# Performance work log

Hardware: AMD Instinct MI355X
Metric: run time of the kernel (lower is better)

Reference implementation:

```python
import jax, jax.numpy as jnp
import numpy as np

_CODESZ = 8   # E8 codeword dimension
_OFFSET = 0.25  # half-integer shift applied to D8 points


def _build_grid():
    # Faithful replication of get_grid(): cartesian product of arange(-4,4)
    # over 8 dims (torch.cartesian_prod order == 'ij' meshgrid, last dim fastest),
    # keep points with even coordinate sum and squared norm <= 10 (D8 subset),
    # then concat [d8 - 1/4, d8 + 1/4]. Yields 55650 codewords of dim 8.
    rng = np.arange(-4, 4, dtype=np.int8)
    pts = np.stack(np.meshgrid(*([rng] * _CODESZ), indexing='ij'), axis=-1).reshape(-1, _CODESZ)
    s = pts.sum(axis=-1, dtype=np.int16)
    n2 = (pts.astype(np.int16) * pts).sum(axis=-1)  # max 8*16 fits int16
    d8 = pts[(s % 2 == 0) & (n2 <= 10)].astype(np.float32)  # [27825, 8]
    grid = np.concatenate([d8 - _OFFSET, d8 + _OFFSET], axis=0)  # [55650, 8]
    grid_norm = (grid * grid).sum(axis=-1)  # diag(grid @ grid.T), [55650]
    return jnp.asarray(grid), jnp.asarray(grid_norm)


def setup_inputs() -> dict:
    key = jax.random.key(0)
    X = jax.random.normal(key, (8192, _CODESZ), dtype=jnp.float32)
    grid, grid_norm = _build_grid()
    return {"X": X, "grid": grid, "grid_norm": grid_norm}


def reference(X, grid, grid_norm):
    # quantize(X, return_idx=True):
    # nearest codeword under L2 <=> argmax of 2*X@g - ||g||^2
    scores = 2.0 * (X @ grid.T) - grid_norm          # [N, 55650]
    idx = jnp.argmax(scores, axis=-1)                # [N]
    vals = jnp.take(grid, idx, axis=0)               # [N, 8]
    idx_i16 = (idx + (-2 ** 15)).astype(jnp.int16)   # idx_offset + int16 cast
    return vals, idx_i16
```

## Files before the change

### kernel.cpp

```cpp
#include <hip/hip_runtime.h>
#include <math.h>


typedef short short8 __attribute__((ext_vector_type(8)));
typedef float f32x16 __attribute__((ext_vector_type(16)));

constexpr int NROWS  = 8192;
constexpr int NCW    = 55650;
constexpr int NT     = 1740;
constexpr int NCWP   = NT * 32;
constexpr int NCHUNK = 24;
constexpr int RBLK   = 32;

constexpr size_t OFF_GB = 0;
constexpr size_t OFF_XS = OFF_GB + (size_t)NCWP * 32;
constexpr size_t OFF_BK = OFF_XS + (size_t)NROWS * 64;

__device__ inline unsigned short bf16_rne(float f) {
  unsigned int u = __float_as_uint(f);
  unsigned int r = u + 0x7FFFu + ((u >> 16) & 1u);
  return (unsigned short)(r >> 16);
}
__device__ inline float bf16_f(unsigned short h) {
  return __uint_as_float(((unsigned int)h) << 16);
}
__device__ inline unsigned int enc_ord(float f) {
  unsigned int u = __float_as_uint(f);
  return (u & 0x80000000u) ? ~u : (u | 0x80000000u);
}
__device__ inline float dec_ord(unsigned int e) {
  unsigned int u = (e & 0x80000000u) ? (e & 0x7FFFFFFFu) : ~e;
  return __uint_as_float(u);
}
__device__ inline float max16(const f32x16& d) {
  float t1 = fmaxf(fmaxf(d[0], d[1]), d[2]);
  float t2 = fmaxf(fmaxf(d[3], d[4]), d[5]);
  float t3 = fmaxf(fmaxf(d[6], d[7]), d[8]);
  float t4 = fmaxf(fmaxf(d[9], d[10]), d[11]);
  float t5 = fmaxf(fmaxf(d[12], d[13]), d[14]);
  float u1 = fmaxf(fmaxf(t1, t2), t3);
  float u2 = fmaxf(fmaxf(t4, t5), d[15]);
  return fmaxf(u1, u2);
}

__global__ __launch_bounds__(256) void e8_prep(
    const float* __restrict__ X, const float* __restrict__ G,
    const float* __restrict__ GN, unsigned short* __restrict__ Gb,
    unsigned short* __restrict__ Xs, unsigned long long* __restrict__ best) {
  int i = blockIdx.x * 256 + threadIdx.x;
  if (i < NCWP) {
    unsigned short g16[16];
    if (i < NCW) {
      for (int j = 0; j < 8; ++j) g16[j] = bf16_rne(G[(size_t)i*8+j]);
      g16[8] = bf16_rne(GN[i]);
      for (int j = 9; j < 16; ++j) g16[j] = 0;
    } else {
      for (int j = 0; j < 8; ++j) g16[j] = 0;
      g16[8] = 0x7F7F;
      for (int j = 9; j < 16; ++j) g16[j] = 0;
    }
    uint4* dst = reinterpret_cast<uint4*>(Gb + (size_t)i * 16);
    dst[0] = *reinterpret_cast<uint4*>(&g16[0]);
    dst[1] = *reinterpret_cast<uint4*>(&g16[8]);
  } else if (i < NCWP + NROWS) {
    int r = i - NCWP;
    unsigned short hh[8], mm[8], ll[8], qq[8];
    for (int j = 0; j < 8; ++j) {
      float s = 2.0f * X[(size_t)r*8+j];
      unsigned short h = bf16_rne(s);  float r1 = s  - bf16_f(h);
      unsigned short m = bf16_rne(r1); float r2 = r1 - bf16_f(m);
      unsigned short l = bf16_rne(r2);
      hh[j] = h; mm[j] = m; ll[j] = l;
      qq[j] = (j == 0) ? (unsigned short)0xBF80 : 0;
    }
    uint4* dst = reinterpret_cast<uint4*>(Xs + (size_t)r * 32);
    dst[0] = *reinterpret_cast<uint4*>(hh);
    dst[1] = *reinterpret_cast<uint4*>(mm);
    dst[2] = *reinterpret_cast<uint4*>(ll);
    dst[3] = *reinterpret_cast<uint4*>(qq);
    best[r] = 0ull;
  }
}

#define E8_ASM(D0, D1, A1, A2)                                             \
  asm volatile(                                                            \
      "v_mfma_f32_32x32x16_bf16 %0, %2, %4, %8\n\t"                        \
      "v_mfma_f32_32x32x16_bf16 %1, %2, %5, %8\n\t"                        \
      "v_mfma_f32_32x32x16_bf16 %0, %3, %6, %0\n\t"                        \
      "v_mfma_f32_32x32x16_bf16 %1, %3, %7, %1\n\t"                        \
      "s_nop 7\n\t"                                                        \
      "s_nop 7"                                                            \
      : "=&v"(D0), "=&v"(D1)                                               \
      : "v"(A1), "v"(A2), "v"(b10), "v"(b11), "v"(b20), "v"(b21), "v"(cz))

#define E8_PIN(P0, P1, T0) asm("" : "+v"(P0), "+v"(P1) : "v"(T0))

#define E8_LOAD(A1, A2)                                                    \
  A1 = *reinterpret_cast<const short8*>(p);                                \
  A2 = *reinterpret_cast<const short8*>(p + koff);                         \
  p += 512;

#define E8_TRACK(D0, D1, TILE)                                             \
  {                                                                        \
    const float m0 = max16(D0);                                            \
    const float m1 = max16(D1);                                            \
    bi0 = (m0 > bs0) ? (TILE) : bi0;  bs0 = fmaxf(bs0, m0);                \
    bi1 = (m1 > bs1) ? (TILE) : bi1;  bs1 = fmaxf(bs1, m1);                \
  }

__global__ __launch_bounds__(256, 3) void e8_main(
    const unsigned short* __restrict__ Gb,
    const unsigned short* __restrict__ Xs,
    unsigned long long* __restrict__ best) {
  const int lane = threadIdx.x & 63;
  const int wave = threadIdx.x >> 6;
  const int kg = lane >> 5, l31 = lane & 31;
  const int rowbase = blockIdx.x * 256 + wave * 64;

  short8 b10, b11, b20, b21;
  {
    const size_t row0 = (size_t)rowbase + l31;
    const size_t row1 = row0 + 32;
    b10 = *reinterpret_cast<const short8*>(Xs + (row0*4 + kg)*8);
    b20 = *reinterpret_cast<const short8*>(Xs + (row0*4 + 2 + kg)*8);
    b11 = *reinterpret_cast<const short8*>(Xs + (row1*4 + kg)*8);
    b21 = *reinterpret_cast<const short8*>(Xs + (row1*4 + 2 + kg)*8);
  }
  asm("" : "+v"(b10), "+v"(b11), "+v"(b20), "+v"(b21));

  const int ct0 = blockIdx.y * NT / NCHUNK;
  const int ct1 = (blockIdx.y + 1) * NT / NCHUNK;

  f32x16 cz;
#pragma unroll
  for (int i = 0; i < 16; ++i) cz[i] = 0.0f;

  float bs0 = -INFINITY, bs1 = -INFINITY;
  int   bi0 = 0,         bi1 = 0;

  const unsigned short* p = Gb + (size_t)ct0 * 512 + (size_t)l31 * 16;
  const int koff = kg << 3;

  short8 aE1, aE2, aO1, aO2;
  f32x16 dE0, dE1, dO0, dO1;

  E8_LOAD(aE1, aE2)
  E8_LOAD(aO1, aO2)
  E8_ASM(dE0, dE1, aE1, aE2);

  int k = ct0 + 1;
  for (; k + 1 < ct1; k += 2) {
    E8_LOAD(aE1, aE2)
    E8_ASM(dO0, dO1, aO1, aO2);
    E8_PIN(dE0, dE1, dO0);
    E8_TRACK(dE0, dE1, k - 1)
    E8_LOAD(aO1, aO2)
    E8_ASM(dE0, dE1, aE1, aE2);
    E8_PIN(dO0, dO1, dE0);
    E8_TRACK(dO0, dO1, k)
  }

  if ((ct1 - ct0 - 1) & 1) {
    E8_ASM(dO0, dO1, aO1, aO2);
    E8_PIN(dE0, dE1, dO0);
    E8_TRACK(dE0, dE1, ct1 - 2)
    E8_TRACK(dO0, dO1, ct1 - 1)
  } else {
    E8_TRACK(dE0, dE1, ct1 - 1)
  }

  {
    unsigned long long key =
        ((unsigned long long)enc_ord(bs0) << 32) | (unsigned int)(~bi0);
    unsigned long long o = __shfl_xor(key, 32, 64);
    key = (o > key) ? o : key;
    if (lane < 32) atomicMax(&best[(size_t)rowbase + l31], key);
  }
  {
    unsigned long long key =
        ((unsigned long long)enc_ord(bs1) << 32) | (unsigned int)(~bi1);
    unsigned long long o = __shfl_xor(key, 32, 64);
    key = (o > key) ? o : key;
    if (lane < 32) atomicMax(&best[(size_t)rowbase + 32 + l31], key);
  }
}

__global__ __launch_bounds__(256) void e8_resolve(
    const unsigned short* __restrict__ Gb,
    const unsigned short* __restrict__ Xs, const float* __restrict__ G,
    const unsigned long long* __restrict__ best, float* __restrict__ out) {
  const int lane = threadIdx.x & 63;
  const int wave = threadIdx.x >> 6;
  const int kg = lane >> 5, l31 = lane & 31;
  const int rt = blockIdx.x;

  short8 b1, b2;
  {
    const size_t row = (size_t)rt * 32 + l31;
    b1 = *reinterpret_cast<const short8*>(Xs + (row*4 + kg)*8);
    b2 = *reinterpret_cast<const short8*>(Xs + (row*4 + 2 + kg)*8);
  }
  f32x16 cz;
#pragma unroll
  for (int i = 0; i < 16; ++i) cz[i] = 0.0f;

  for (int j = wave * 8; j < wave * 8 + 8; ++j) {
    const int srow = rt * 32 + j;
    const unsigned long long k = best[srow];
    const float sstar = dec_ord((unsigned int)(k >> 32));
    const int twin = (int)(~(unsigned int)(k & 0xFFFFFFFFull));

    const unsigned short* ga = Gb + (size_t)twin * 512 + (size_t)l31 * 16;
    short8 a1 = *reinterpret_cast<const short8*>(ga);
    short8 a2 = *reinterpret_cast<const short8*>(ga + (kg << 3));
    f32x16 d = __builtin_amdgcn_mfma_f32_32x32x16_bf16(a1, b1, cz, 0, 0, 0);
    d = __builtin_amdgcn_mfma_f32_32x32x16_bf16(a2, b2, d, 0, 0, 0);

    const int base = twin * 32 + 4 * kg;
    int cand = 0x7FFFFFFF;
#pragma unroll
    for (int r = 15; r >= 0; --r)
      cand = (d[r] == sstar) ? (base + ((r & 3) + 8 * (r >> 2))) : cand;
    if (l31 != j) cand = 0x7FFFFFFF;
    const int o = __shfl_xor(cand, 32, 64);
    cand = min(cand, o);
    if (lane == j) {
      const float4* g = reinterpret_cast<const float4*>(G + (size_t)cand * 8);
      float4 v0 = g[0], v1 = g[1];
      float4* od = reinterpret_cast<float4*>(out + (size_t)srow * 8);
      od[0] = v0; od[1] = v1;
      out[(size_t)NROWS * 8 + srow] = (float)(cand - 32768);
    }
  }
}

extern "C" void kernel_launch(void* const* d_in, const int* in_sizes, int n_in,
                              void* d_out, int out_size, void* d_ws, size_t ws_size,
                              hipStream_t stream) {
  const float* X  = (const float*)d_in[0];
  const float* G  = (const float*)d_in[1];
  const float* GN = (const float*)d_in[2];
  float* out = (float*)d_out;

  char* ws = (char*)d_ws;
  unsigned short*     Gb   = (unsigned short*)(ws + OFF_GB);
  unsigned short*     Xs   = (unsigned short*)(ws + OFF_XS);
  unsigned long long* best = (unsigned long long*)(ws + OFF_BK);

  e8_prep<<<(NCWP + NROWS + 255) / 256, 256, 0, stream>>>(X, G, GN, Gb, Xs, best);
  e8_main<<<dim3(RBLK, NCHUNK), 256, 0, stream>>>(Gb, Xs, best);
  e8_resolve<<<256, 256, 0, stream>>>(Gb, Xs, G, best, out);
}
```

Before: 43.58 us.

## Stage codeword tiles through double-buffered LDS shared by all waves

The main kernel now loads codeword tiles cooperatively into a double-buffered shared-memory staging area, 16 tiles per batch. The global loads for the next batch are issued into registers before the current batch's MFMAs and written to LDS afterwards. The codeword buffer is also relaid out as a split 1KB-per-tile format (coordinates in one half, norms in the other) so tiles copy contiguously. This replaces the per-wave redundant global loads, since all 4 waves read the same tiles, with one shared load per block. In exchange it adds a __syncthreads per batch, 32KB of LDS (which may limit occupancy at 3 blocks per CU), and extra VGPRs for the staged values.

```diff
diff --git a/kernel.cpp b/kernel.cpp
--- a/kernel.cpp
+++ b/kernel.cpp
@@ -4,6 +4,7 @@
 
 typedef short short8 __attribute__((ext_vector_type(8)));
 typedef float f32x16 __attribute__((ext_vector_type(16)));
+typedef unsigned int u32x4 __attribute__((ext_vector_type(4)));
 
 constexpr int NROWS  = 8192;
 constexpr int NCW    = 55650;
@@ -11,9 +12,10 @@
 constexpr int NCWP   = NT * 32;
 constexpr int NCHUNK = 24;
 constexpr int RBLK   = 32;
+constexpr int NB     = 16;
 
 constexpr size_t OFF_GB = 0;
-constexpr size_t OFF_XS = OFF_GB + (size_t)NCWP * 32;
+constexpr size_t OFF_XS = OFF_GB + (size_t)NT * 1024;
 constexpr size_t OFF_BK = OFF_XS + (size_t)NROWS * 64;
 
 __device__ inline unsigned short bf16_rne(float f) {
@@ -45,23 +47,23 @@
 
 __global__ __launch_bounds__(256) void e8_prep(
     const float* __restrict__ X, const float* __restrict__ G,
-    const float* __restrict__ GN, unsigned short* __restrict__ Gb,
+    const float* __restrict__ GN, unsigned char* __restrict__ GbB,
     unsigned short* __restrict__ Xs, unsigned long long* __restrict__ best) {
   int i = blockIdx.x * 256 + threadIdx.x;
   if (i < NCWP) {
-    unsigned short g16[16];
+    unsigned short c8[8], n8[8];
     if (i < NCW) {
-      for (int j = 0; j < 8; ++j) g16[j] = bf16_rne(G[(size_t)i*8+j]);
-      g16[8] = bf16_rne(GN[i]);
-      for (int j = 9; j < 16; ++j) g16[j] = 0;
+      for (int j = 0; j < 8; ++j) c8[j] = bf16_rne(G[(size_t)i*8+j]);
+      n8[0] = bf16_rne(GN[i]);
+      for (int j = 1; j < 8; ++j) n8[j] = 0;
     } else {
-      for (int j = 0; j < 8; ++j) g16[j] = 0;
-      g16[8] = 0x7F7F;
-      for (int j = 9; j < 16; ++j) g16[j] = 0;
-    }
-    uint4* dst = reinterpret_cast<uint4*>(Gb + (size_t)i * 16);
-    dst[0] = *reinterpret_cast<uint4*>(&g16[0]);
-    dst[1] = *reinterpret_cast<uint4*>(&g16[8]);
+      for (int j = 0; j < 8; ++j) c8[j] = 0;
+      n8[0] = 0x7F7F;
+      for (int j = 1; j < 8; ++j) n8[j] = 0;
+    }
+    unsigned char* base = GbB + (size_t)(i >> 5) * 1024 + (size_t)(i & 31) * 16;
+    *reinterpret_cast<u32x4*>(base)       = *reinterpret_cast<u32x4*>(c8);
+    *reinterpret_cast<u32x4*>(base + 512) = *reinterpret_cast<u32x4*>(n8);
   } else if (i < NCWP + NROWS) {
     int r = i - NCWP;
     unsigned short hh[8], mm[8], ll[8], qq[8];
@@ -73,11 +75,11 @@
       hh[j] = h; mm[j] = m; ll[j] = l;
       qq[j] = (j == 0) ? (unsigned short)0xBF80 : 0;
     }
-    uint4* dst = reinterpret_cast<uint4*>(Xs + (size_t)r * 32);
-    dst[0] = *reinterpret_cast<uint4*>(hh);
-    dst[1] = *reinterpret_cast<uint4*>(mm);
-    dst[2] = *reinterpret_cast<uint4*>(ll);
-    dst[3] = *reinterpret_cast<uint4*>(qq);
+    u32x4* dst = reinterpret_cast<u32x4*>(Xs + (size_t)r * 32);
+    dst[0] = *reinterpret_cast<u32x4*>(hh);
+    dst[1] = *reinterpret_cast<u32x4*>(mm);
+    dst[2] = *reinterpret_cast<u32x4*>(ll);
+    dst[3] = *reinterpret_cast<u32x4*>(qq);
     best[r] = 0ull;
   }
 }
@@ -95,11 +97,6 @@
 
 #define E8_PIN(P0, P1, T0) asm("" : "+v"(P0), "+v"(P1) : "v"(T0))
 
-#define E8_LOAD(A1, A2)                                                    \
-  A1 = *reinterpret_cast<const short8*>(p);                                \
-  A2 = *reinterpret_cast<const short8*>(p + koff);                         \
-  p += 512;
-
 #define E8_TRACK(D0, D1, TILE)                                             \
   {                                                                        \
     const float m0 = max16(D0);                                            \
@@ -108,14 +105,22 @@
     bi1 = (m1 > bs1) ? (TILE) : bi1;  bs1 = fmaxf(bs1, m1);                \
   }
 
+#define E8_LDSA(A1, A2, TL)                                                \
+  A1 = *reinterpret_cast<const short8*>(lb + (TL) * 1024 + l31 * 16);      \
+  A2 = *reinterpret_cast<const short8*>(lb + (TL) * 1024 + kgoff + l31 * 16);
+
 __global__ __launch_bounds__(256, 3) void e8_main(
-    const unsigned short* __restrict__ Gb,
+    const unsigned char* __restrict__ GbB,
     const unsigned short* __restrict__ Xs,
     unsigned long long* __restrict__ best) {
   const int lane = threadIdx.x & 63;
   const int wave = threadIdx.x >> 6;
   const int kg = lane >> 5, l31 = lane & 31;
+  const int kgoff = kg << 9;
   const int rowbase = blockIdx.x * 256 + wave * 64;
+
+  __shared__ u32x4 smem4[2048];
+  unsigned char* smemB = reinterpret_cast<unsigned char*>(smem4);
 
   short8 b10, b11, b20, b21;
   {
@@ -138,35 +143,86 @@
   float bs0 = -INFINITY, bs1 = -INFINITY;
   int   bi0 = 0,         bi1 = 0;
 
-  const unsigned short* p = Gb + (size_t)ct0 * 512 + (size_t)l31 * 16;
-  const int koff = kg << 3;
-
-  short8 aE1, aE2, aO1, aO2;
-  f32x16 dE0, dE1, dO0, dO1;
-
-  E8_LOAD(aE1, aE2)
-  E8_LOAD(aO1, aO2)
-  E8_ASM(dE0, dE1, aE1, aE2);
-
-  int k = ct0 + 1;
-  for (; k + 1 < ct1; k += 2) {
-    E8_LOAD(aE1, aE2)
-    E8_ASM(dO0, dO1, aO1, aO2);
-    E8_PIN(dE0, dE1, dO0);
-    E8_TRACK(dE0, dE1, k - 1)
-    E8_LOAD(aO1, aO2)
+  {
+    const int cnt0 = (ct1 - ct0 < NB) ? (ct1 - ct0) : NB;
+#pragma unroll
+    for (int t = 0; t < 4; ++t) {
+      const int widx = wave * 4 + t;
+      if (widx < cnt0) {
+        u32x4 v = *reinterpret_cast<const u32x4*>(
+            GbB + (size_t)(ct0 + widx) * 1024 + (size_t)lane * 16);
+        *reinterpret_cast<u32x4*>(smemB + (size_t)widx * 1024 +
+                                  (size_t)lane * 16) = v;
+      }
+    }
+  }
+  __syncthreads();
+
+  int base = ct0, bufsel = 0;
+  while (base < ct1) {
+    const int cnt   = (ct1 - base < NB) ? (ct1 - base) : NB;
+    const int nbase = base + cnt;
+    const int ncnt  = (ct1 - nbase < NB) ? (ct1 - nbase) : NB;
+
+    u32x4 sv0 = {0,0,0,0}, sv1 = {0,0,0,0}, sv2 = {0,0,0,0}, sv3 = {0,0,0,0};
+#pragma unroll
+    for (int t = 0; t < 4; ++t) {
+      const int widx = wave * 4 + t;
+      u32x4 v = {0, 0, 0, 0};
+      if (widx < ncnt)
+        v = *reinterpret_cast<const u32x4*>(
+            GbB + (size_t)(nbase + widx) * 1024 + (size_t)lane * 16);
+      if (t == 0) sv0 = v; else if (t == 1) sv1 = v;
+      else if (t == 2) sv2 = v; else sv3 = v;
+    }
+    asm("" : "+v"(sv0), "+v"(sv1), "+v"(sv2), "+v"(sv3));
+
+    const unsigned char* lb = smemB + (size_t)bufsel * 16384;
+    short8 aE1, aE2, aO1, aO2;
+    f32x16 dE0, dE1, dO0, dO1;
+
+    E8_LDSA(aE1, aE2, 0)
+    if (cnt > 1) { E8_LDSA(aO1, aO2, 1) }
     E8_ASM(dE0, dE1, aE1, aE2);
-    E8_PIN(dO0, dO1, dE0);
-    E8_TRACK(dO0, dO1, k)
-  }
-
-  if ((ct1 - ct0 - 1) & 1) {
-    E8_ASM(dO0, dO1, aO1, aO2);
-    E8_PIN(dE0, dE1, dO0);
-    E8_TRACK(dE0, dE1, ct1 - 2)
-    E8_TRACK(dO0, dO1, ct1 - 1)
-  } else {
-    E8_TRACK(dE0, dE1, ct1 - 1)
+
+    int i = 1;
+    for (; i + 1 < cnt; i += 2) {
+      {
+        const int pt = i + 1;
+        E8_LDSA(aE1, aE2, pt)
+        E8_ASM(dO0, dO1, aO1, aO2);
+        E8_PIN(dE0, dE1, dO0);
+        E8_TRACK(dE0, dE1, base + i - 1)
+      }
+      {
+        const int pt = (i + 2 < cnt) ? i + 2 : 0;
+        E8_LDSA(aO1, aO2, pt)
+        E8_ASM(dE0, dE1, aE1, aE2);
+        E8_PIN(dO0, dO1, dE0);
+        E8_TRACK(dO0, dO1, base + i)
+      }
+    }
+    if (i < cnt) {
+      E8_ASM(dO0, dO1, aO1, aO2);
+      E8_PIN(dE0, dE1, dO0);
+      E8_TRACK(dE0, dE1, base + i - 1)
+      E8_TRACK(dO0, dO1, base + i)
+    } else {
+      E8_TRACK(dE0, dE1, base + cnt - 1)
+    }
+
+#pragma unroll
+    for (int t = 0; t < 4; ++t) {
+      const int widx = wave * 4 + t;
+      if (widx < ncnt) {
+        const u32x4 v = (t == 0) ? sv0 : (t == 1) ? sv1 : (t == 2) ? sv2 : sv3;
+        *reinterpret_cast<u32x4*>(smemB + (size_t)(bufsel ^ 1) * 16384 +
+                                  (size_t)widx * 1024 + (size_t)lane * 16) = v;
+      }
+    }
+    __syncthreads();
+    bufsel ^= 1;
+    base = nbase;
   }
 
   {
@@ -186,7 +242,7 @@
 }
 
 __global__ __launch_bounds__(256) void e8_resolve(
-    const unsigned short* __restrict__ Gb,
+    const unsigned char* __restrict__ GbB,
     const unsigned short* __restrict__ Xs, const float* __restrict__ G,
     const unsigned long long* __restrict__ best, float* __restrict__ out) {
   const int lane = threadIdx.x & 63;
@@ -210,17 +266,17 @@
     const float sstar = dec_ord((unsigned int)(k >> 32));
     const int twin = (int)(~(unsigned int)(k & 0xFFFFFFFFull));
 
-    const unsigned short* ga = Gb + (size_t)twin * 512 + (size_t)l31 * 16;
+    const unsigned char* ga = GbB + (size_t)twin * 1024 + (size_t)l31 * 16;
     short8 a1 = *reinterpret_cast<const short8*>(ga);
-    short8 a2 = *reinterpret_cast<const short8*>(ga + (kg << 3));
+    short8 a2 = *reinterpret_cast<const short8*>(ga + (kg << 9));
     f32x16 d = __builtin_amdgcn_mfma_f32_32x32x16_bf16(a1, b1, cz, 0, 0, 0);
     d = __builtin_amdgcn_mfma_f32_32x32x16_bf16(a2, b2, d, 0, 0, 0);
 
-    const int base = twin * 32 + 4 * kg;
+    const int basei = twin * 32 + 4 * kg;
     int cand = 0x7FFFFFFF;
 #pragma unroll
     for (int r = 15; r >= 0; --r)
-      cand = (d[r] == sstar) ? (base + ((r & 3) + 8 * (r >> 2))) : cand;
+      cand = (d[r] == sstar) ? (basei + ((r & 3) + 8 * (r >> 2))) : cand;
     if (l31 != j) cand = 0x7FFFFFFF;
     const int o = __shfl_xor(cand, 32, 64);
     cand = min(cand, o);
@@ -243,11 +299,11 @@
   float* out = (float*)d_out;
 
   char* ws = (char*)d_ws;
-  unsigned short*     Gb   = (unsigned short*)(ws + OFF_GB);
+  unsigned char*      GbB  = (unsigned char*)(ws + OFF_GB);
   unsigned short*     Xs   = (unsigned short*)(ws + OFF_XS);
   unsigned long long* best = (unsigned long long*)(ws + OFF_BK);
 
-  e8_prep<<<(NCWP + NROWS + 255) / 256, 256, 0, stream>>>(X, G, GN, Gb, Xs, best);
-  e8_main<<<dim3(RBLK, NCHUNK), 256, 0, stream>>>(Gb, Xs, best);
-  e8_resolve<<<256, 256, 0, stream>>>(Gb, Xs, G, best, out);
-}
+  e8_prep<<<(NCWP + NROWS + 255) / 256, 256, 0, stream>>>(X, G, GN, GbB, Xs, best);
+  e8_main<<<dim3(RBLK, NCHUNK), 256, 0, stream>>>(GbB, Xs, best);
+  e8_resolve<<<256, 256, 0, stream>>>(GbB, Xs, G, best, out);
+}
```

Result: slower. 46.66 us (+7.1%).
